# Performance work log

Measured on AMD Instinct MI355X. Metric: run time of the kernel, lower is better.

The kernel has to match this reference:

```python
import jax, jax.numpy as jnp
import numpy as np

L, P = 8, 512
HID = 128
N_COARSE, N_FINE = 64, 128
LVIS_NEAR, LVIS_FAR = 1e-3, 0.5
S = 100.0  # 1 / fixed_s_recp


def _mlp_sdf(x, w0, b0, w1, b1, w2, b2, w3, b3):
    # x: [..., 3] -> sdf [...]
    h = jax.nn.relu(x @ w0 + b0)
    h = jax.nn.relu(h @ w1 + b1)
    h = jax.nn.relu(h @ w2 + b2)
    return (h @ w3 + b3)[..., 0]


def _sdf_to_w(sdf, s):
    # faithful to sdf_to_w: cdf -> alpha -> visibility weights via cumprod
    cdf = jax.nn.sigmoid(sdf * s)
    alpha = jnp.clip((cdf[..., :-1] - cdf[..., 1:]) / (cdf[..., :-1] + 1e-10), 0.0, None)
    ones = jnp.ones(alpha.shape[:-1] + (1,), alpha.dtype)
    shifted = jnp.concatenate([ones, 1.0 - alpha + 1e-10], axis=-1)
    return alpha * jnp.cumprod(shifted, axis=-1)[..., :-1]


def _sample_pdf(bins, weights, u):
    # standard NeRF importance sampling; bins [...,M+1], weights [...,M], u [...,N]
    weights = weights + 1e-5
    pdf = weights / jnp.sum(weights, axis=-1, keepdims=True)
    cdf = jnp.cumsum(pdf, axis=-1)
    cdf = jnp.concatenate([jnp.zeros_like(cdf[..., :1]), cdf], axis=-1)  # [...,M+1]
    # searchsorted (right) via broadcast compare: [...,N,M+1]
    inds = jnp.sum((u[..., None] >= cdf[..., None, :]).astype(jnp.int32), axis=-1)
    below = jnp.clip(inds - 1, 0, cdf.shape[-1] - 1)
    above = jnp.clip(inds, 0, cdf.shape[-1] - 1)
    cdf_b = jnp.take_along_axis(cdf, below, axis=-1)
    cdf_a = jnp.take_along_axis(cdf, above, axis=-1)
    bins_b = jnp.take_along_axis(bins, below, axis=-1)
    bins_a = jnp.take_along_axis(bins, above, axis=-1)
    denom = cdf_a - cdf_b
    denom = jnp.where(denom < 1e-5, jnp.ones_like(denom), denom)
    t = (u - cdf_b) / denom
    return bins_b + t * (bins_a - bins_b)


def setup_inputs() -> dict:
    key = jax.random.key(0)
    ks = jax.random.split(key, 8)

    def lin(k, fi, fo):
        return jax.random.normal(k, (fi, fo), jnp.float32) / jnp.sqrt(jnp.float32(fi))

    return {
        "pts": jax.random.normal(ks[0], (1, P, 3), jnp.float32) * 0.5,
        "light_posi": jax.random.normal(ks[1], (L, 3), jnp.float32) * 2.0,
        "u": jax.random.uniform(ks[2], (L, P, N_FINE), jnp.float32),
        "w0": lin(ks[3], 3, HID), "b0": jnp.zeros((HID,), jnp.float32),
        "w1": lin(ks[4], HID, HID), "b1": jnp.zeros((HID,), jnp.float32),
        "w2": lin(ks[5], HID, HID), "b2": jnp.zeros((HID,), jnp.float32),
        "w3": lin(ks[6], HID, 1), "b3": jnp.zeros((1,), jnp.float32),
    }


def reference(pts, light_posi, u, w0, b0, w1, b1, w2, b2, w3, b3):
    sdf = lambda x: _mlp_sdf(x, w0, b0, w1, b1, w2, b2, w3, b3)
    # pts: [1,P,3]; light_posi: [L,3]
    pts2l = light_posi[:, None, :] - pts  # [L,P,3]
    pts2l = pts2l / jnp.linalg.norm(pts2l, axis=-1, keepdims=True)
    t = jnp.linspace(0.0, 1.0 - 1.0 / N_COARSE, N_COARSE, dtype=jnp.float32)
    d_coarse = LVIS_NEAR * (1.0 - t) + LVIS_FAR * t  # [N_COARSE]
    d_coarse = jnp.broadcast_to(d_coarse, (pts2l.shape[0], pts.shape[1], N_COARSE))
    # coarse sample points: [L,P,Nc,3]
    pts_coarse = pts[:, :, None, :] + d_coarse[..., None] * pts2l[:, :, None, :]
    w_coarse = _sdf_to_w(sdf(pts_coarse), S)  # [L,P,Nc-1]
    d_fine = _sample_pdf(d_coarse, w_coarse, u)  # [L,P,Nf]
    d_all = jnp.sort(jnp.concatenate([d_coarse, d_fine], axis=-1), axis=-1)  # [L,P,Nc+Nf]
    pts_all = pts[:, :, None, :] + d_all[..., None] * pts2l[:, :, None, :]
    w_all = _sdf_to_w(sdf(pts_all), S)
    occu = jnp.sum(w_all, axis=-1)  # [L,P]
    return 1.0 - occu
```

## Files before the change

### kernel.cpp

```cpp
#include <hip/hip_runtime.h>
#include <math.h>

#define NL 8
#define NP 512
#define NC 64
#define NF 128
#define NALL 192
#define NRAY (NL * NP)
#define HID 128

typedef _Float16 half8 __attribute__((ext_vector_type(8)));
typedef _Float16 half4v __attribute__((ext_vector_type(4)));
typedef float floatx16 __attribute__((ext_vector_type(16)));
typedef unsigned long long ull;

#define MFMA(a, b, c) __builtin_amdgcn_mfma_f32_32x32x16_f16((a), (b), (c), 0, 0, 0)

__device__ __forceinline__ float dcoarse_at(int i) {
    float t = (float)i * 0.015625f;
    return 1e-3f * (1.0f - t) + 0.5f * t;
}

__device__ __forceinline__ floatx16 fzero16() {
    floatx16 z;
#pragma unroll
    for (int i = 0; i < 16; ++i) z[i] = 0.f;
    return z;
}
__device__ __forceinline__ half8 hzero8() {
    half8 z;
#pragma unroll
    for (int i = 0; i < 8; ++i) z[i] = (_Float16)0.f;
    return z;
}

__global__ void prep_kernel(const float* __restrict__ w1, const float* __restrict__ w2,
                            _Float16* __restrict__ Wsp) {
    int f = blockIdx.x * 256 + threadIdx.x;
    int layer = blockIdx.y;
    const float* w = layer ? w2 : w1;
    int i = f & 7, l31 = (f >> 3) & 31, lhi = (f >> 8) & 1, ks = (f >> 9) & 7, jb = f >> 12;
    int j = jb * 32 + l31;
    int k = ks * 16 + lhi * 8 + i;
    float v = w[k * 128 + j];
    _Float16 hi = (_Float16)v;
    Wsp[(layer * 2 + 0) * 16384 + f] = hi;
    Wsp[(layer * 2 + 1) * 16384 + f] = (_Float16)(v - (float)hi);
}

template<int MODE, int FASTW>
__global__ __launch_bounds__(256, 2) void mlp_kernel(
    const float* __restrict__ pts, const float* __restrict__ lights,
    const float* __restrict__ d_fine,
    const float* __restrict__ w0, const float* __restrict__ b0,
    const float* __restrict__ w1, const float* __restrict__ b1,
    const float* __restrict__ w2, const float* __restrict__ b2,
    const float* __restrict__ w3, const float* __restrict__ b3,
    const _Float16* __restrict__ Wsp,
    float* __restrict__ sdf_out)
{
    __shared__ __align__(16) _Float16 Hhi[128 * 128];
    __shared__ __align__(16) _Float16 Hlo[128 * 128];
    __shared__ _Float16 Xs[6 * 128];
    __shared__ float P2[2 * 128];

    const int tid = threadIdx.x;
    const int lane = tid & 63;
    const int wv = tid >> 6;
    const int jh = wv & 1, mh = wv >> 1;
    const int l31 = lane & 31, lhi = lane >> 5;
    const int base = blockIdx.x * 128;

    if (tid < 128) {
        int pt = base + tid;
        int ray; float d;
        if (MODE == 0) { ray = pt >> 6; d = dcoarse_at(pt & 63); }
        else           { ray = pt >> 7; d = d_fine[pt]; }
        int l = ray >> 9, p = ray & (NP - 1);
        float px = pts[p * 3 + 0], py = pts[p * 3 + 1], pz = pts[p * 3 + 2];
        float dx = lights[l * 3 + 0] - px, dy = lights[l * 3 + 1] - py, dz = lights[l * 3 + 2] - pz;
        float n = sqrtf(dx * dx + dy * dy + dz * dz);
        dx /= n; dy /= n; dz /= n;
        float xc[3] = { px + d * dx, py + d * dy, pz + d * dz };
#pragma unroll
        for (int c = 0; c < 3; ++c) {
            _Float16 h = (_Float16)xc[c];
            Xs[c * 128 + tid] = h;
            Xs[(3 + c) * 128 + tid] = (_Float16)(xc[c] - (float)h);
        }
    }
    __syncthreads();

    const int m0 = mh * 64;

    auto haddr = [&](int m, int k0) {
        return m * 128 + ((((k0 >> 3) ^ (m & 15)) << 3) | (k0 & 7));
    };

    auto store_tile = [&](const floatx16& a, int jt, int mt, const float* __restrict__ bias) {
        int m = m0 + mt * 32 + l31;
#pragma unroll
        for (int g = 0; g < 4; ++g) {
            int jg = jh * 64 + jt * 32 + 8 * g + 4 * lhi;
            half4v hq, lq;
#pragma unroll
            for (int q = 0; q < 4; ++q) {
                float v = fmaxf(a[g * 4 + q] + bias[jg + q], 0.f);
                _Float16 hi = (_Float16)v;
                hq[q] = hi;
                lq[q] = (_Float16)(v - (float)hi);
            }
            int ad = haddr(m, jg);
            *(half4v*)&Hhi[ad] = hq;
            *(half4v*)&Hlo[ad] = lq;
        }
    };

    floatx16 acc[2][2];

    {
        half8 a1h[2], a1l[2], bh1[2], bl1[2];
#pragma unroll
        for (int jt = 0; jt < 2; ++jt) { a1h[jt] = hzero8(); a1l[jt] = hzero8(); }
#pragma unroll
        for (int mt = 0; mt < 2; ++mt) { bh1[mt] = hzero8(); bl1[mt] = hzero8(); }
        if (lhi == 0) {
#pragma unroll
            for (int jt = 0; jt < 2; ++jt) {
                int j = jh * 64 + jt * 32 + l31;
#pragma unroll
                for (int c = 0; c < 3; ++c) {
                    float v = w0[c * 128 + j];
                    _Float16 hi = (_Float16)v;
                    a1h[jt][c] = hi;
                    a1l[jt][c] = (_Float16)(v - (float)hi);
                }
            }
#pragma unroll
            for (int mt = 0; mt < 2; ++mt) {
                int m = m0 + mt * 32 + l31;
#pragma unroll
                for (int c = 0; c < 3; ++c) {
                    bh1[mt][c] = Xs[c * 128 + m];
                    bl1[mt][c] = Xs[(3 + c) * 128 + m];
                }
            }
        }
#pragma unroll
        for (int jt = 0; jt < 2; ++jt)
#pragma unroll
            for (int mt = 0; mt < 2; ++mt) acc[jt][mt] = fzero16();
#pragma unroll
        for (int jt = 0; jt < 2; ++jt)
#pragma unroll
            for (int mt = 0; mt < 2; ++mt) acc[jt][mt] = MFMA(a1l[jt], bh1[mt], acc[jt][mt]);
#pragma unroll
        for (int jt = 0; jt < 2; ++jt)
#pragma unroll
            for (int mt = 0; mt < 2; ++mt) acc[jt][mt] = MFMA(a1h[jt], bl1[mt], acc[jt][mt]);
#pragma unroll
        for (int jt = 0; jt < 2; ++jt)
#pragma unroll
            for (int mt = 0; mt < 2; ++mt) acc[jt][mt] = MFMA(a1h[jt], bh1[mt], acc[jt][mt]);
#pragma unroll
        for (int jt = 0; jt < 2; ++jt)
#pragma unroll
            for (int mt = 0; mt < 2; ++mt) store_tile(acc[jt][mt], jt, mt, b0);
    }
    __syncthreads();

    auto ldA = [&](int L, int jt, int ks, half8& ah, half8& al) {
        if (FASTW) {
            int off = ((((jh * 2 + jt) * 8 + ks) * 2 + lhi) * 32 + l31) * 8;
            ah = *(const half8*)&Wsp[(L * 2 + 0) * 16384 + off];
            al = *(const half8*)&Wsp[(L * 2 + 1) * 16384 + off];
        } else {
            const float* w = L ? w2 : w1;
            int j = jh * 64 + jt * 32 + l31, k0 = ks * 16 + lhi * 8;
#pragma unroll
            for (int i = 0; i < 8; ++i) {
                float v = w[(k0 + i) * 128 + j];
                _Float16 hi = (_Float16)v;
                ah[i] = hi;
                al[i] = (_Float16)(v - (float)hi);
            }
        }
    };

    half8 bh[2][8], bl[2][8];

    auto gemm = [&](int L) {
#pragma unroll
        for (int mt = 0; mt < 2; ++mt) {
            int m = m0 + mt * 32 + l31;
#pragma unroll
            for (int ks = 0; ks < 8; ++ks) {
                int ad = haddr(m, ks * 16 + lhi * 8);
                bh[mt][ks] = *(const half8*)&Hhi[ad];
                bl[mt][ks] = *(const half8*)&Hlo[ad];
            }
        }
#pragma unroll
        for (int jt = 0; jt < 2; ++jt)
#pragma unroll
            for (int mt = 0; mt < 2; ++mt) acc[jt][mt] = fzero16();
#pragma unroll
        for (int ks = 0; ks < 8; ++ks) {
            half8 ah[2], al[2];
            ldA(L, 0, ks, ah[0], al[0]);
            ldA(L, 1, ks, ah[1], al[1]);
#pragma unroll
            for (int jt = 0; jt < 2; ++jt)
#pragma unroll
                for (int mt = 0; mt < 2; ++mt) acc[jt][mt] = MFMA(al[jt], bh[mt][ks], acc[jt][mt]);
#pragma unroll
            for (int jt = 0; jt < 2; ++jt)
#pragma unroll
                for (int mt = 0; mt < 2; ++mt) acc[jt][mt] = MFMA(ah[jt], bl[mt][ks], acc[jt][mt]);
#pragma unroll
            for (int jt = 0; jt < 2; ++jt)
#pragma unroll
                for (int mt = 0; mt < 2; ++mt) acc[jt][mt] = MFMA(ah[jt], bh[mt][ks], acc[jt][mt]);
        }
    };

    gemm(0);
    __syncthreads();
#pragma unroll
    for (int jt = 0; jt < 2; ++jt)
#pragma unroll
        for (int mt = 0; mt < 2; ++mt) store_tile(acc[jt][mt], jt, mt, b1);
    __syncthreads();

    gemm(1);
#pragma unroll
    for (int mt = 0; mt < 2; ++mt) {
        float p = 0.f;
#pragma unroll
        for (int jt = 0; jt < 2; ++jt)
#pragma unroll
            for (int g = 0; g < 4; ++g) {
                int jg = jh * 64 + jt * 32 + 8 * g + 4 * lhi;
#pragma unroll
                for (int q = 0; q < 4; ++q) {
                    float v = fmaxf(acc[jt][mt][g * 4 + q] + b2[jg + q], 0.f);
                    p = fmaf(v, w3[jg + q], p);
                }
            }
        p += __shfl_xor(p, 32);
        if (lane < 32) P2[jh * 128 + m0 + mt * 32 + l31] = p;
    }
    __syncthreads();
    if (tid < 128) sdf_out[base + tid] = b3[0] + P2[tid] + P2[128 + tid];
}

__global__ __launch_bounds__(256) void sample_kernel(
    const float* __restrict__ sdf_c, const float* __restrict__ u,
    float* __restrict__ d_fine, unsigned char* __restrict__ perm8) {
    const int lane = threadIdx.x & 63, wv = threadIdx.x >> 6;
    const int ray = blockIdx.x * 4 + wv;

    float sv = sdf_c[ray * NC + lane];
    float c = 1.0f / (1.0f + expf(-100.0f * sv));
    float cn = __shfl_down(c, 1);
    bool valid = lane < 63;
    float a = valid ? fmaxf((c - cn) / (c + 1e-10f), 0.f) : 0.f;
    float sh = valid ? (1.f - a + 1e-10f) : 1.f;
    float ps = sh;
#pragma unroll
    for (int off = 1; off < 64; off <<= 1) { float o = __shfl_up(ps, off); if (lane >= off) ps *= o; }
    float T = __shfl_up(ps, 1);
    if (lane == 0) T = 1.f;
    float w = valid ? (a * T + 1e-5f) : 0.f;
    float wsum = w;
#pragma unroll
    for (int off = 1; off < 64; off <<= 1) wsum += __shfl_xor(wsum, off);
    float pdf = w / wsum;
    float cs = pdf;
#pragma unroll
    for (int off = 1; off < 64; off <<= 1) { float o = __shfl_up(cs, off); if (lane >= off) cs += o; }
    float cdfv = __shfl_up(cs, 1);
    if (lane == 0) cdfv = 0.f;

    float df[2];
#pragma unroll
    for (int t = 0; t < 2; ++t) {
        float uu = u[ray * NF + t * 64 + lane];
        int lo = 0;
#pragma unroll
        for (int b = 32; b >= 1; b >>= 1) {
            float cm = __shfl(cdfv, lo + b);
            if (uu >= cm) lo += b;
        }
        int above = min(lo + 1, NC - 1);
        float cb = __shfl(cdfv, lo), ca = __shfl(cdfv, above);
        float bb = dcoarse_at(lo), ba = dcoarse_at(above);
        float denom = ca - cb;
        if (denom < 1e-5f) denom = 1.f;
        float tt = (uu - cb) / denom;
        df[t] = bb + tt * (ba - bb);
        d_fine[ray * 128 + t * 64 + lane] = df[t];
    }

    ull v[4];
    v[0] = ((ull)__float_as_uint(dcoarse_at(lane)) << 32) | (unsigned)lane;
    v[1] = ((ull)__float_as_uint(df[0]) << 32) | (unsigned)(64 + lane);
    v[2] = ((ull)__float_as_uint(df[1]) << 32) | (unsigned)(128 + lane);
    v[3] = ((ull)0x7F800000u << 32) | 255u;
    for (int k = 2; k <= 256; k <<= 1) {
        for (int j = k >> 1; j > 0; j >>= 1) {
            if (j >= 64) {
                int tj = j >> 6;
#pragma unroll
                for (int t = 0; t < 4; ++t) {
                    if ((t & tj) == 0) {
                        int t2 = t ^ tj;
                        bool asc = (((t * 64) & k) == 0);
                        ull x = v[t], y = v[t2];
                        bool sw = asc ? (x > y) : (x < y);
                        if (sw) { v[t] = y; v[t2] = x; }
                    }
                }
            } else {
#pragma unroll
                for (int t = 0; t < 4; ++t) {
                    int i = t * 64 + lane;
                    ull other = __shfl_xor(v[t], j);
                    bool lower = (lane & j) == 0;
                    bool asc = ((i & k) == 0);
                    bool takeMin = (lower == asc);
                    ull mn = v[t] < other ? v[t] : other;
                    ull mx = v[t] < other ? other : v[t];
                    v[t] = takeMin ? mn : mx;
                }
            }
        }
    }
#pragma unroll
    for (int t = 0; t < 3; ++t)
        perm8[ray * NALL + t * 64 + lane] = (unsigned char)(v[t] & 0xFFu);
}

__global__ __launch_bounds__(256) void finish_kernel(
    const float* __restrict__ sdf_c, const float* __restrict__ sdf_f,
    const unsigned char* __restrict__ perm8, float* __restrict__ out) {
    int lane = threadIdx.x & 63, wv = threadIdx.x >> 6;
    int ray = blockIdx.x * 4 + wv;
    const unsigned char* P = perm8 + (size_t)ray * NALL;
    float c[4];
#pragma unroll
    for (int t = 0; t < 4; ++t) {
        int i = lane * 3 + t;
        if (i < NALL) {
            int idx = P[i];
            float s = (idx < 64) ? sdf_c[ray * NC + idx] : sdf_f[ray * 128 + (idx - 64)];
            c[t] = 1.0f / (1.0f + expf(-100.0f * s));
        } else c[t] = 0.f;
    }
    float a[3], s[3];
#pragma unroll
    for (int t = 0; t < 3; ++t) {
        int i = lane * 3 + t;
        if (i < NALL - 1) {
            a[t] = fmaxf((c[t] - c[t + 1]) / (c[t] + 1e-10f), 0.f);
            s[t] = 1.f - a[t] + 1e-10f;
        } else { a[t] = 0.f; s[t] = 1.f; }
    }
    float chunk = s[0] * s[1] * s[2];
    float ps = chunk;
#pragma unroll
    for (int off = 1; off < 64; off <<= 1) {
        float o = __shfl_up(ps, off);
        if (lane >= off) ps *= o;
    }
    float T = __shfl_up(ps, 1);
    if (lane == 0) T = 1.f;
    float occ = a[0] * T;
    T *= s[0]; occ = fmaf(a[1], T, occ);
    T *= s[1]; occ = fmaf(a[2], T, occ);
#pragma unroll
    for (int off = 1; off < 64; off <<= 1) occ += __shfl_xor(occ, off);
    if (lane == 0) out[ray] = 1.f - occ;
}

extern "C" void kernel_launch(void* const* d_in, const int* in_sizes, int n_in,
                              void* d_out, int out_size, void* d_ws, size_t ws_size,
                              hipStream_t stream) {
    const float* pts = (const float*)d_in[0];
    const float* lights = (const float*)d_in[1];
    const float* u = (const float*)d_in[2];
    const float* w0 = (const float*)d_in[3];
    const float* b0 = (const float*)d_in[4];
    const float* w1 = (const float*)d_in[5];
    const float* b1 = (const float*)d_in[6];
    const float* w2 = (const float*)d_in[7];
    const float* b2 = (const float*)d_in[8];
    const float* w3 = (const float*)d_in[9];
    const float* b3 = (const float*)d_in[10];
    float* out = (float*)d_out;

    char* wsb = (char*)d_ws;
    float* sdf_c = (float*)wsb;
    float* sdf_f = (float*)(wsb + (size_t)NRAY * NC * 4);
    float* d_fine = (float*)(wsb + (size_t)NRAY * (NC + 128) * 4);
    unsigned char* perm8 = (unsigned char*)(wsb + (size_t)NRAY * (NC + 256) * 4);
    _Float16* Wsp = (_Float16*)(wsb + (size_t)NRAY * (NC + 256) * 4 + (size_t)NRAY * NALL);
    const size_t need = (size_t)NRAY * (NC + 256) * 4 + (size_t)NRAY * NALL
                      + (size_t)4 * 16384 * sizeof(_Float16);
    const bool fast = ws_size >= need;

    if (fast) {
        prep_kernel<<<dim3(64, 2), 256, 0, stream>>>(w1, w2, Wsp);
        mlp_kernel<0, 1><<<(NRAY * NC) / 128, 256, 0, stream>>>(
            pts, lights, nullptr, w0, b0, w1, b1, w2, b2, w3, b3, Wsp, sdf_c);
        sample_kernel<<<NRAY / 4, 256, 0, stream>>>(sdf_c, u, d_fine, perm8);
        mlp_kernel<1, 1><<<(NRAY * 128) / 128, 256, 0, stream>>>(
            pts, lights, d_fine, w0, b0, w1, b1, w2, b2, w3, b3, Wsp, sdf_f);
    } else {
        mlp_kernel<0, 0><<<(NRAY * NC) / 128, 256, 0, stream>>>(
            pts, lights, nullptr, w0, b0, w1, b1, w2, b2, w3, b3, nullptr, sdf_c);
        sample_kernel<<<NRAY / 4, 256, 0, stream>>>(sdf_c, u, d_fine, perm8);
        mlp_kernel<1, 0><<<(NRAY * 128) / 128, 256, 0, stream>>>(
            pts, lights, d_fine, w0, b0, w1, b1, w2, b2, w3, b3, nullptr, sdf_f);
    }
    finish_kernel<<<NRAY / 4, 256, 0, stream>>>(sdf_c, sdf_f, perm8, out);
}
```

Before: 253.3 us.

## Share one LDS activation buffer between hi and lo halves in two passes

Drops the separate hi and lo fp16 activation buffers in shared memory in favour of a single buffer. Each layer's GEMM now runs in two passes: first with the hi activations (the A-lo and A-hi products), then with the lo activations, which are held packed in registers until written after a barrier. This halves LDS use (aiming at more resident blocks) and no longer preloads all B fragments into registers, at the cost of extra barriers and staged stores, plus reloading the hi weights in the second pass.

```diff
diff --git a/kernel.cpp b/kernel.cpp
--- a/kernel.cpp
+++ b/kernel.cpp
@@ -33,6 +33,12 @@
     for (int i = 0; i < 8; ++i) z[i] = (_Float16)0.f;
     return z;
 }
+__device__ __forceinline__ unsigned pack2(_Float16 a, _Float16 b) {
+    union { _Float16 h[2]; unsigned u; } P;
+    P.h[0] = a; P.h[1] = b;
+    return P.u;
+}
+union H4U { half4v v; unsigned u[2]; };
 
 __global__ void prep_kernel(const float* __restrict__ w1, const float* __restrict__ w2,
                             _Float16* __restrict__ Wsp) {
@@ -59,8 +65,7 @@
     const _Float16* __restrict__ Wsp,
     float* __restrict__ sdf_out)
 {
-    __shared__ __align__(16) _Float16 Hhi[128 * 128];
-    __shared__ __align__(16) _Float16 Hlo[128 * 128];
+    __shared__ __align__(16) _Float16 H[128 * 128];
     __shared__ _Float16 Xs[6 * 128];
     __shared__ float P2[2 * 128];
 
@@ -97,26 +102,39 @@
         return m * 128 + ((((k0 >> 3) ^ (m & 15)) << 3) | (k0 & 7));
     };
 
-    auto store_tile = [&](const floatx16& a, int jt, int mt, const float* __restrict__ bias) {
+    floatx16 acc[2][2];
+    unsigned lohold[2][2][4][2];
+
+    auto store_hi = [&](int jt, int mt, const float* __restrict__ bias) {
         int m = m0 + mt * 32 + l31;
 #pragma unroll
         for (int g = 0; g < 4; ++g) {
             int jg = jh * 64 + jt * 32 + 8 * g + 4 * lhi;
-            half4v hq, lq;
+            half4v hq;
+            _Float16 lo[4];
 #pragma unroll
             for (int q = 0; q < 4; ++q) {
-                float v = fmaxf(a[g * 4 + q] + bias[jg + q], 0.f);
+                float v = fmaxf(acc[jt][mt][g * 4 + q] + bias[jg + q], 0.f);
                 _Float16 hi = (_Float16)v;
                 hq[q] = hi;
-                lq[q] = (_Float16)(v - (float)hi);
-            }
-            int ad = haddr(m, jg);
-            *(half4v*)&Hhi[ad] = hq;
-            *(half4v*)&Hlo[ad] = lq;
-        }
-    };
-
-    floatx16 acc[2][2];
+                lo[q] = (_Float16)(v - (float)hi);
+            }
+            lohold[jt][mt][g][0] = pack2(lo[0], lo[1]);
+            lohold[jt][mt][g][1] = pack2(lo[2], lo[3]);
+            *(half4v*)&H[haddr(m, jg)] = hq;
+        }
+    };
+    auto store_lo = [&](int jt, int mt) {
+        int m = m0 + mt * 32 + l31;
+#pragma unroll
+        for (int g = 0; g < 4; ++g) {
+            int jg = jh * 64 + jt * 32 + 8 * g + 4 * lhi;
+            H4U u;
+            u.u[0] = lohold[jt][mt][g][0];
+            u.u[1] = lohold[jt][mt][g][1];
+            *(half4v*)&H[haddr(m, jg)] = u.v;
+        }
+    };
 
     {
         half8 a1h[2], a1l[2], bh1[2], bl1[2];
@@ -165,11 +183,11 @@
 #pragma unroll
         for (int jt = 0; jt < 2; ++jt)
 #pragma unroll
-            for (int mt = 0; mt < 2; ++mt) store_tile(acc[jt][mt], jt, mt, b0);
-    }
-    __syncthreads();
-
-    auto ldA = [&](int L, int jt, int ks, half8& ah, half8& al) {
+            for (int mt = 0; mt < 2; ++mt) store_hi(jt, mt, b0);
+    }
+    __syncthreads();
+
+    auto ldA2 = [&](int L, int jt, int ks, half8& ah, half8& al) {
         if (FASTW) {
             int off = ((((jh * 2 + jt) * 8 + ks) * 2 + lhi) * 32 + l31) * 8;
             ah = *(const half8*)&Wsp[(L * 2 + 0) * 16384 + off];
@@ -186,53 +204,81 @@
             }
         }
     };
-
-    half8 bh[2][8], bl[2][8];
-
-    auto gemm = [&](int L) {
-#pragma unroll
-        for (int mt = 0; mt < 2; ++mt) {
-            int m = m0 + mt * 32 + l31;
-#pragma unroll
-            for (int ks = 0; ks < 8; ++ks) {
-                int ad = haddr(m, ks * 16 + lhi * 8);
-                bh[mt][ks] = *(const half8*)&Hhi[ad];
-                bl[mt][ks] = *(const half8*)&Hlo[ad];
-            }
-        }
+    auto ldAh = [&](int L, int jt, int ks, half8& ah) {
+        if (FASTW) {
+            int off = ((((jh * 2 + jt) * 8 + ks) * 2 + lhi) * 32 + l31) * 8;
+            ah = *(const half8*)&Wsp[(L * 2 + 0) * 16384 + off];
+        } else {
+            const float* w = L ? w2 : w1;
+            int j = jh * 64 + jt * 32 + l31, k0 = ks * 16 + lhi * 8;
+#pragma unroll
+            for (int i = 0; i < 8; ++i) ah[i] = (_Float16)w[(k0 + i) * 128 + j];
+        }
+    };
+
+    auto passA = [&](int L) {
 #pragma unroll
         for (int jt = 0; jt < 2; ++jt)
 #pragma unroll
             for (int mt = 0; mt < 2; ++mt) acc[jt][mt] = fzero16();
 #pragma unroll
         for (int ks = 0; ks < 8; ++ks) {
-            half8 ah[2], al[2];
-            ldA(L, 0, ks, ah[0], al[0]);
-            ldA(L, 1, ks, ah[1], al[1]);
+            half8 ah[2], al[2], b[2];
+            ldA2(L, 0, ks, ah[0], al[0]);
+            ldA2(L, 1, ks, ah[1], al[1]);
+#pragma unroll
+            for (int mt = 0; mt < 2; ++mt)
+                b[mt] = *(const half8*)&H[haddr(m0 + mt * 32 + l31, ks * 16 + lhi * 8)];
 #pragma unroll
             for (int jt = 0; jt < 2; ++jt)
 #pragma unroll
-                for (int mt = 0; mt < 2; ++mt) acc[jt][mt] = MFMA(al[jt], bh[mt][ks], acc[jt][mt]);
+                for (int mt = 0; mt < 2; ++mt) acc[jt][mt] = MFMA(al[jt], b[mt], acc[jt][mt]);
 #pragma unroll
             for (int jt = 0; jt < 2; ++jt)
 #pragma unroll
-                for (int mt = 0; mt < 2; ++mt) acc[jt][mt] = MFMA(ah[jt], bl[mt][ks], acc[jt][mt]);
+                for (int mt = 0; mt < 2; ++mt) acc[jt][mt] = MFMA(ah[jt], b[mt], acc[jt][mt]);
+        }
+    };
+    auto passB = [&](int L) {
+#pragma unroll
+        for (int ks = 0; ks < 8; ++ks) {
+            half8 ah[2], b[2];
+            ldAh(L, 0, ks, ah[0]);
+            ldAh(L, 1, ks, ah[1]);
+#pragma unroll
+            for (int mt = 0; mt < 2; ++mt)
+                b[mt] = *(const half8*)&H[haddr(m0 + mt * 32 + l31, ks * 16 + lhi * 8)];
 #pragma unroll
             for (int jt = 0; jt < 2; ++jt)
 #pragma unroll
-                for (int mt = 0; mt < 2; ++mt) acc[jt][mt] = MFMA(ah[jt], bh[mt][ks], acc[jt][mt]);
-        }
-    };
-
-    gemm(0);
+                for (int mt = 0; mt < 2; ++mt) acc[jt][mt] = MFMA(ah[jt], b[mt], acc[jt][mt]);
+        }
+    };
+
+    passA(0);
     __syncthreads();
 #pragma unroll
     for (int jt = 0; jt < 2; ++jt)
 #pragma unroll
-        for (int mt = 0; mt < 2; ++mt) store_tile(acc[jt][mt], jt, mt, b1);
-    __syncthreads();
-
-    gemm(1);
+        for (int mt = 0; mt < 2; ++mt) store_lo(jt, mt);
+    __syncthreads();
+    passB(0);
+    __syncthreads();
+#pragma unroll
+    for (int jt = 0; jt < 2; ++jt)
+#pragma unroll
+        for (int mt = 0; mt < 2; ++mt) store_hi(jt, mt, b1);
+    __syncthreads();
+
+    passA(1);
+    __syncthreads();
+#pragma unroll
+    for (int jt = 0; jt < 2; ++jt)
+#pragma unroll
+        for (int mt = 0; mt < 2; ++mt) store_lo(jt, mt);
+    __syncthreads();
+    passB(1);
+
 #pragma unroll
     for (int mt = 0; mt < 2; ++mt) {
         float p = 0.f;
```

Measured after the change: 283.9 us. +12.1%, slower.

## Fuse importance sampling and final compositing into the MLP kernels

Applied to the files above, without the earlier changes.

The sample kernel is folded into the coarse MLP kernel's epilogue, with each block of 128 coarse points covering two rays. The finish kernel is folded into the fine MLP kernel's epilogue, reading fine SDF values from shared memory. This removes two launches and the global round trip of sdf_f. In exchange, only one or two of four waves do the serial epilogue work while the others sit idle, which lengthens each block's tail.

```diff
diff --git a/kernel.cpp b/kernel.cpp
--- a/kernel.cpp
+++ b/kernel.cpp
@@ -51,13 +51,14 @@
 template<int MODE, int FASTW>
 __global__ __launch_bounds__(256, 2) void mlp_kernel(
     const float* __restrict__ pts, const float* __restrict__ lights,
-    const float* __restrict__ d_fine,
+    const float* __restrict__ u,
+    float* __restrict__ d_fine, unsigned char* __restrict__ perm8,
     const float* __restrict__ w0, const float* __restrict__ b0,
     const float* __restrict__ w1, const float* __restrict__ b1,
     const float* __restrict__ w2, const float* __restrict__ b2,
     const float* __restrict__ w3, const float* __restrict__ b3,
     const _Float16* __restrict__ Wsp,
-    float* __restrict__ sdf_out)
+    float* __restrict__ sdf_c, float* __restrict__ out)
 {
     __shared__ __align__(16) _Float16 Hhi[128 * 128];
     __shared__ __align__(16) _Float16 Hlo[128 * 128];
@@ -251,136 +252,136 @@
         if (lane < 32) P2[jh * 128 + m0 + mt * 32 + l31] = p;
     }
     __syncthreads();
-    if (tid < 128) sdf_out[base + tid] = b3[0] + P2[tid] + P2[128 + tid];
-}
-
-__global__ __launch_bounds__(256) void sample_kernel(
-    const float* __restrict__ sdf_c, const float* __restrict__ u,
-    float* __restrict__ d_fine, unsigned char* __restrict__ perm8) {
-    const int lane = threadIdx.x & 63, wv = threadIdx.x >> 6;
-    const int ray = blockIdx.x * 4 + wv;
-
-    float sv = sdf_c[ray * NC + lane];
-    float c = 1.0f / (1.0f + expf(-100.0f * sv));
-    float cn = __shfl_down(c, 1);
-    bool valid = lane < 63;
-    float a = valid ? fmaxf((c - cn) / (c + 1e-10f), 0.f) : 0.f;
-    float sh = valid ? (1.f - a + 1e-10f) : 1.f;
-    float ps = sh;
-#pragma unroll
-    for (int off = 1; off < 64; off <<= 1) { float o = __shfl_up(ps, off); if (lane >= off) ps *= o; }
-    float T = __shfl_up(ps, 1);
-    if (lane == 0) T = 1.f;
-    float w = valid ? (a * T + 1e-5f) : 0.f;
-    float wsum = w;
-#pragma unroll
-    for (int off = 1; off < 64; off <<= 1) wsum += __shfl_xor(wsum, off);
-    float pdf = w / wsum;
-    float cs = pdf;
-#pragma unroll
-    for (int off = 1; off < 64; off <<= 1) { float o = __shfl_up(cs, off); if (lane >= off) cs += o; }
-    float cdfv = __shfl_up(cs, 1);
-    if (lane == 0) cdfv = 0.f;
-
-    float df[2];
-#pragma unroll
-    for (int t = 0; t < 2; ++t) {
-        float uu = u[ray * NF + t * 64 + lane];
-        int lo = 0;
-#pragma unroll
-        for (int b = 32; b >= 1; b >>= 1) {
-            float cm = __shfl(cdfv, lo + b);
-            if (uu >= cm) lo += b;
-        }
-        int above = min(lo + 1, NC - 1);
-        float cb = __shfl(cdfv, lo), ca = __shfl(cdfv, above);
-        float bb = dcoarse_at(lo), ba = dcoarse_at(above);
-        float denom = ca - cb;
-        if (denom < 1e-5f) denom = 1.f;
-        float tt = (uu - cb) / denom;
-        df[t] = bb + tt * (ba - bb);
-        d_fine[ray * 128 + t * 64 + lane] = df[t];
-    }
-
-    ull v[4];
-    v[0] = ((ull)__float_as_uint(dcoarse_at(lane)) << 32) | (unsigned)lane;
-    v[1] = ((ull)__float_as_uint(df[0]) << 32) | (unsigned)(64 + lane);
-    v[2] = ((ull)__float_as_uint(df[1]) << 32) | (unsigned)(128 + lane);
-    v[3] = ((ull)0x7F800000u << 32) | 255u;
-    for (int k = 2; k <= 256; k <<= 1) {
-        for (int j = k >> 1; j > 0; j >>= 1) {
-            if (j >= 64) {
-                int tj = j >> 6;
-#pragma unroll
-                for (int t = 0; t < 4; ++t) {
-                    if ((t & tj) == 0) {
-                        int t2 = t ^ tj;
-                        bool asc = (((t * 64) & k) == 0);
-                        ull x = v[t], y = v[t2];
-                        bool sw = asc ? (x > y) : (x < y);
-                        if (sw) { v[t] = y; v[t2] = x; }
+    if (tid < 128) {
+        float s = b3[0] + P2[tid] + P2[128 + tid];
+        if (MODE == 0) sdf_c[base + tid] = s;
+        P2[tid] = s;
+    }
+    __syncthreads();
+
+    if (MODE == 0) {
+        if (wv < 2) {
+            const int ray = blockIdx.x * 2 + wv;
+            float sv = P2[wv * 64 + lane];
+            float c = 1.0f / (1.0f + expf(-100.0f * sv));
+            float cn = __shfl_down(c, 1);
+            bool valid = lane < 63;
+            float a = valid ? fmaxf((c - cn) / (c + 1e-10f), 0.f) : 0.f;
+            float sh = valid ? (1.f - a + 1e-10f) : 1.f;
+            float ps = sh;
+#pragma unroll
+            for (int off = 1; off < 64; off <<= 1) { float o = __shfl_up(ps, off); if (lane >= off) ps *= o; }
+            float T = __shfl_up(ps, 1);
+            if (lane == 0) T = 1.f;
+            float w = valid ? (a * T + 1e-5f) : 0.f;
+            float wsum = w;
+#pragma unroll
+            for (int off = 1; off < 64; off <<= 1) wsum += __shfl_xor(wsum, off);
+            float pdf = w / wsum;
+            float cs = pdf;
+#pragma unroll
+            for (int off = 1; off < 64; off <<= 1) { float o = __shfl_up(cs, off); if (lane >= off) cs += o; }
+            float cdfv = __shfl_up(cs, 1);
+            if (lane == 0) cdfv = 0.f;
+
+            float df[2];
+#pragma unroll
+            for (int t = 0; t < 2; ++t) {
+                float uu = u[ray * NF + t * 64 + lane];
+                int lo = 0;
+#pragma unroll
+                for (int b = 32; b >= 1; b >>= 1) {
+                    float cm = __shfl(cdfv, lo + b);
+                    if (uu >= cm) lo += b;
+                }
+                int above = min(lo + 1, NC - 1);
+                float cb = __shfl(cdfv, lo), ca = __shfl(cdfv, above);
+                float bb = dcoarse_at(lo), ba = dcoarse_at(above);
+                float denom = ca - cb;
+                if (denom < 1e-5f) denom = 1.f;
+                float tt = (uu - cb) / denom;
+                df[t] = bb + tt * (ba - bb);
+                d_fine[ray * 128 + t * 64 + lane] = df[t];
+            }
+
+            ull v[4];
+            v[0] = ((ull)__float_as_uint(dcoarse_at(lane)) << 32) | (unsigned)lane;
+            v[1] = ((ull)__float_as_uint(df[0]) << 32) | (unsigned)(64 + lane);
+            v[2] = ((ull)__float_as_uint(df[1]) << 32) | (unsigned)(128 + lane);
+            v[3] = ((ull)0x7F800000u << 32) | 255u;
+            for (int k = 2; k <= 256; k <<= 1) {
+                for (int j = k >> 1; j > 0; j >>= 1) {
+                    if (j >= 64) {
+                        int tj = j >> 6;
+#pragma unroll
+                        for (int t = 0; t < 4; ++t) {
+                            if ((t & tj) == 0) {
+                                int t2 = t ^ tj;
+                                bool asc = (((t * 64) & k) == 0);
+                                ull x = v[t], y = v[t2];
+                                bool sw = asc ? (x > y) : (x < y);
+                                if (sw) { v[t] = y; v[t2] = x; }
+                            }
+                        }
+                    } else {
+#pragma unroll
+                        for (int t = 0; t < 4; ++t) {
+                            int i = t * 64 + lane;
+                            ull other = __shfl_xor(v[t], j);
+                            bool lower = (lane & j) == 0;
+                            bool asc = ((i & k) == 0);
+                            bool takeMin = (lower == asc);
+                            ull mn = v[t] < other ? v[t] : other;
+                            ull mx = v[t] < other ? other : v[t];
+                            v[t] = takeMin ? mn : mx;
+                        }
                     }
                 }
-            } else {
-#pragma unroll
-                for (int t = 0; t < 4; ++t) {
-                    int i = t * 64 + lane;
-                    ull other = __shfl_xor(v[t], j);
-                    bool lower = (lane & j) == 0;
-                    bool asc = ((i & k) == 0);
-                    bool takeMin = (lower == asc);
-                    ull mn = v[t] < other ? v[t] : other;
-                    ull mx = v[t] < other ? other : v[t];
-                    v[t] = takeMin ? mn : mx;
-                }
-            }
-        }
-    }
-#pragma unroll
-    for (int t = 0; t < 3; ++t)
-        perm8[ray * NALL + t * 64 + lane] = (unsigned char)(v[t] & 0xFFu);
-}
-
-__global__ __launch_bounds__(256) void finish_kernel(
-    const float* __restrict__ sdf_c, const float* __restrict__ sdf_f,
-    const unsigned char* __restrict__ perm8, float* __restrict__ out) {
-    int lane = threadIdx.x & 63, wv = threadIdx.x >> 6;
-    int ray = blockIdx.x * 4 + wv;
-    const unsigned char* P = perm8 + (size_t)ray * NALL;
-    float c[4];
-#pragma unroll
-    for (int t = 0; t < 4; ++t) {
-        int i = lane * 3 + t;
-        if (i < NALL) {
-            int idx = P[i];
-            float s = (idx < 64) ? sdf_c[ray * NC + idx] : sdf_f[ray * 128 + (idx - 64)];
-            c[t] = 1.0f / (1.0f + expf(-100.0f * s));
-        } else c[t] = 0.f;
-    }
-    float a[3], s[3];
-#pragma unroll
-    for (int t = 0; t < 3; ++t) {
-        int i = lane * 3 + t;
-        if (i < NALL - 1) {
-            a[t] = fmaxf((c[t] - c[t + 1]) / (c[t] + 1e-10f), 0.f);
-            s[t] = 1.f - a[t] + 1e-10f;
-        } else { a[t] = 0.f; s[t] = 1.f; }
-    }
-    float chunk = s[0] * s[1] * s[2];
-    float ps = chunk;
-#pragma unroll
-    for (int off = 1; off < 64; off <<= 1) {
-        float o = __shfl_up(ps, off);
-        if (lane >= off) ps *= o;
-    }
-    float T = __shfl_up(ps, 1);
-    if (lane == 0) T = 1.f;
-    float occ = a[0] * T;
-    T *= s[0]; occ = fmaf(a[1], T, occ);
-    T *= s[1]; occ = fmaf(a[2], T, occ);
-#pragma unroll
-    for (int off = 1; off < 64; off <<= 1) occ += __shfl_xor(occ, off);
-    if (lane == 0) out[ray] = 1.f - occ;
+            }
+#pragma unroll
+            for (int t = 0; t < 3; ++t)
+                perm8[ray * NALL + t * 64 + lane] = (unsigned char)(v[t] & 0xFFu);
+        }
+    } else {
+        if (wv == 0) {
+            const int ray = blockIdx.x;
+            const unsigned char* P = perm8 + (size_t)ray * NALL;
+            float c[4];
+#pragma unroll
+            for (int t = 0; t < 4; ++t) {
+                int i = lane * 3 + t;
+                if (i < NALL) {
+                    int idx = P[i];
+                    float s = (idx < 64) ? sdf_c[ray * NC + idx] : P2[idx - 64];
+                    c[t] = 1.0f / (1.0f + expf(-100.0f * s));
+                } else c[t] = 0.f;
+            }
+            float a[3], s[3];
+#pragma unroll
+            for (int t = 0; t < 3; ++t) {
+                int i = lane * 3 + t;
+                if (i < NALL - 1) {
+                    a[t] = fmaxf((c[t] - c[t + 1]) / (c[t] + 1e-10f), 0.f);
+                    s[t] = 1.f - a[t] + 1e-10f;
+                } else { a[t] = 0.f; s[t] = 1.f; }
+            }
+            float chunk = s[0] * s[1] * s[2];
+            float ps = chunk;
+#pragma unroll
+            for (int off = 1; off < 64; off <<= 1) {
+                float o = __shfl_up(ps, off);
+                if (lane >= off) ps *= o;
+            }
+            float T = __shfl_up(ps, 1);
+            if (lane == 0) T = 1.f;
+            float occ = a[0] * T;
+            T *= s[0]; occ = fmaf(a[1], T, occ);
+            T *= s[1]; occ = fmaf(a[2], T, occ);
+#pragma unroll
+            for (int off = 1; off < 64; off <<= 1) occ += __shfl_xor(occ, off);
+            if (lane == 0) out[ray] = 1.f - occ;
+        }
+    }
 }
 
 extern "C" void kernel_launch(void* const* d_in, const int* in_sizes, int n_in,
@@ -401,27 +402,27 @@
 
     char* wsb = (char*)d_ws;
     float* sdf_c = (float*)wsb;
-    float* sdf_f = (float*)(wsb + (size_t)NRAY * NC * 4);
-    float* d_fine = (float*)(wsb + (size_t)NRAY * (NC + 128) * 4);
-    unsigned char* perm8 = (unsigned char*)(wsb + (size_t)NRAY * (NC + 256) * 4);
-    _Float16* Wsp = (_Float16*)(wsb + (size_t)NRAY * (NC + 256) * 4 + (size_t)NRAY * NALL);
-    const size_t need = (size_t)NRAY * (NC + 256) * 4 + (size_t)NRAY * NALL
+    float* d_fine = (float*)(wsb + (size_t)NRAY * NC * 4);
+    unsigned char* perm8 = (unsigned char*)(wsb + (size_t)NRAY * (NC + 128) * 4);
+    _Float16* Wsp = (_Float16*)(wsb + (size_t)NRAY * (NC + 128) * 4 + (size_t)NRAY * NALL);
+    const size_t need = (size_t)NRAY * (NC + 128) * 4 + (size_t)NRAY * NALL
                       + (size_t)4 * 16384 * sizeof(_Float16);
     const bool fast = ws_size >= need;
 
     if (fast) {
         prep_kernel<<<dim3(64, 2), 256, 0, stream>>>(w1, w2, Wsp);
         mlp_kernel<0, 1><<<(NRAY * NC) / 128, 256, 0, stream>>>(
-            pts, lights, nullptr, w0, b0, w1, b1, w2, b2, w3, b3, Wsp, sdf_c);
-        sample_kernel<<<NRAY / 4, 256, 0, stream>>>(sdf_c, u, d_fine, perm8);
-        mlp_kernel<1, 1><<<(NRAY * 128) / 128, 256, 0, stream>>>(
-            pts, lights, d_fine, w0, b0, w1, b1, w2, b2, w3, b3, Wsp, sdf_f);
+            pts, lights, u, d_fine, perm8,
+            w0, b0, w1, b1, w2, b2, w3, b3, Wsp, sdf_c, out);
+        mlp_kernel<1, 1><<<NRAY, 256, 0, stream>>>(
+            pts, lights, u, d_fine, perm8,
+            w0, b0, w1, b1, w2, b2, w3, b3, Wsp, sdf_c, out);
     } else {
         mlp_kernel<0, 0><<<(NRAY * NC) / 128, 256, 0, stream>>>(
-            pts, lights, nullptr, w0, b0, w1, b1, w2, b2, w3, b3, nullptr, sdf_c);
-        sample_kernel<<<NRAY / 4, 256, 0, stream>>>(sdf_c, u, d_fine, perm8);
-        mlp_kernel<1, 0><<<(NRAY * 128) / 128, 256, 0, stream>>>(
-            pts, lights, d_fine, w0, b0, w1, b1, w2, b2, w3, b3, nullptr, sdf_f);
-    }
-    finish_kernel<<<NRAY / 4, 256, 0, stream>>>(sdf_c, sdf_f, perm8, out);
-}
+            pts, lights, u, d_fine, perm8,
+            w0, b0, w1, b1, w2, b2, w3, b3, nullptr, sdf_c, out);
+        mlp_kernel<1, 0><<<NRAY, 256, 0, stream>>>(
+            pts, lights, u, d_fine, perm8,
+            w0, b0, w1, b1, w2, b2, w3, b3, nullptr, sdf_c, out);
+    }
+}
```

After: 279.4 us. +10.3%, slower.
